# Kernel tuning notes

Measured on AMD Instinct MI355X. Metric: run time of the kernel, lower is better.

The kernel has to match this reference:

```python
import jax, jax.numpy as jnp
import numpy as np

B, N = 65536, 32
Z = jnp.array([0.0, 0.0, 1.0], dtype=jnp.float32)  # joint rotation axis
G = 9.81  # gravity magnitude along +z of base frame (matches base_lin_acc[:,2]=9.81)


def skew(v):
    # [..., 3] -> [..., 3, 3] skew-symmetric matrix
    x, y, z = v[..., 0], v[..., 1], v[..., 2]
    o = jnp.zeros_like(x)
    return jnp.stack([jnp.stack([o, -z, y], -1),
                      jnp.stack([z, o, -x], -1),
                      jnp.stack([-y, x, o], -1)], -2)


def rot_z(q):
    # [B] -> [B, 3, 3] rotation about z (revolute joint)
    c, s = jnp.cos(q), jnp.sin(q)
    o, l = jnp.zeros_like(q), jnp.ones_like(q)
    return jnp.stack([jnp.stack([c, -s, o], -1),
                      jnp.stack([s, c, o], -1),
                      jnp.stack([o, o, l], -1)], -2)


def setup_inputs() -> dict:
    key = jax.random.key(0)
    ks = jax.random.split(key, 8)
    return {
        "q": jax.random.normal(ks[0], (B, N), jnp.float32),
        "qd": jax.random.normal(ks[1], (B, N), jnp.float32),
        "qdd_des": jax.random.normal(ks[2], (B, N), jnp.float32),
        "trans": jax.random.uniform(ks[3], (N, 3), jnp.float32),      # fixed joint-origin offsets
        "mass": jax.random.uniform(ks[4], (N,), jnp.float32) + 0.1,   # positive link masses
        "com": jax.random.uniform(ks[5], (N, 3), jnp.float32),        # center of mass per link
        "inertia": jax.random.normal(ks[6], (N, 3, 3), jnp.float32),  # rotational inertia (about CoM)
        "damping": jax.random.uniform(ks[7], (N,), jnp.float32),      # joint damping consts
    }


def reference(q, qd, qdd_des, trans, mass, com, inertia, damping):
    """Recursive Newton-Euler inverse dynamics (compute_inverse_dynamics),
    for a serial chain of N revolute-z joints, include_gravity=True."""
    Bn = q.shape[0]
    mcom = mass[:, None] * com                                        # [N,3]
    S = skew(com)                                                     # [N,3,3]
    # spatial inertia: I + m * skew(c) @ skew(c)^T (multiply_motion_vec)
    Ibar = inertia + mass[:, None, None] * (S @ jnp.swapaxes(S, -1, -2))

    def fwd_step(carry, xs):
        # propagate velocity/acceleration from parent into child body frame
        v_lin, v_ang, a_lin, a_ang = carry
        qj, qdj, qddj, p = xs
        R = rot_z(qj)                                                 # joint_pose rotation [B,3,3]
        Rt = jnp.swapaxes(R, -1, -2)
        t = -jnp.einsum('bij,j->bi', Rt, p)                           # inverse() translation
        # SpatialMotionVec.transform: ang' = R ang ; lin' = t x ang' + R lin
        wv = jnp.einsum('bij,bj->bi', Rt, v_ang)
        lv = jnp.cross(t, wv) + jnp.einsum('bij,bj->bi', Rt, v_lin)
        wa = jnp.einsum('bij,bj->bi', Rt, a_ang)
        la = jnp.cross(t, wa) + jnp.einsum('bij,bj->bi', Rt, a_lin)
        jv = qdj[:, None] * Z                                         # joint_vel (ang only)
        ja = qddj[:, None] * Z                                        # joint_acc (ang only)
        v_ang_n = wv + jv
        v_lin_n = lv
        # acc = parent_acc + joint_acc + vel x joint_vel (cross_motion_vec)
        a_ang_n = wa + ja + jnp.cross(v_ang_n, jv)
        a_lin_n = la + jnp.cross(v_lin_n, jv)
        c = (v_lin_n, v_ang_n, a_lin_n, a_ang_n)
        return c, (v_lin_n, v_ang_n, a_lin_n, a_ang_n, R)

    zeros3 = jnp.zeros((Bn, 3), q.dtype)
    base_lin_acc = zeros3.at[:, 2].set(jnp.asarray(G, q.dtype))       # gravity as base acc
    init = (zeros3, zeros3, base_lin_acc, zeros3)
    xs = (q.T, qd.T, qdd_des.T, trans)
    _, (v_lin_s, v_ang_s, a_lin_s, a_ang_s, R_s) = jax.lax.scan(fwd_step, init, xs)

    def bwd_step(carry, xs):
        # backward force recursion: f_i = I a_i + v_i x* (I v_i) + X(joint_pose_{i+1}) f_{i+1}
        g_lin, g_ang = carry
        v_lin, v_ang, a_lin, a_ang, R, p, m, mc, Ib = xs
        # inertia.multiply_motion_vec on acc and vel
        fa_lin = m * a_lin + jnp.cross(mc[None, :], a_ang)
        fa_ang = jnp.einsum('ij,bj->bi', Ib, a_ang) + jnp.cross(mc[None, :], a_lin)
        fv_lin = m * v_lin + jnp.cross(mc[None, :], v_ang)
        fv_ang = jnp.einsum('ij,bj->bi', Ib, v_ang) + jnp.cross(mc[None, :], v_lin)
        # vel.cross_force_vec(I v)
        cf_ang = jnp.cross(v_ang, fv_ang) + jnp.cross(v_lin, fv_lin)
        cf_lin = jnp.cross(v_ang, fv_lin)
        f_lin = fa_lin + cf_lin + g_lin
        f_ang = fa_ang + cf_ang + g_ang
        tau = f_ang[:, 2]                                             # force.ang . z_axis
        # SpatialForceVec.transform by this body's joint_pose (into parent frame)
        Rf = jnp.einsum('bij,bj->bi', R, f_lin)
        out_ang = jnp.cross(p[None, :], Rf) + jnp.einsum('bij,bj->bi', R, f_ang)
        return (Rf, out_ang), tau

    xs_b = (v_lin_s, v_ang_s, a_lin_s, a_ang_s, R_s, trans, mass, mcom, Ibar)
    _, taus = jax.lax.scan(bwd_step, (zeros3, zeros3), xs_b, reverse=True)
    # taus: [N, B]; add joint damping term: damping * qd
    return taus.T + damping[None, :] * qd
```

## Files before the change

### kernel.cpp

```cpp
#include <hip/hip_runtime.h>

#define NJ 32
#define BLK 256

typedef float f2 __attribute__((ext_vector_type(2)));
__device__ __forceinline__ f2 mk2(float x, float y){ f2 r; r.x=x; r.y=y; return r; }


#define MODS1 "row_shr:1 row_mask:0xf bank_mask:0xf bound_ctrl:0"
#define MODS2 "row_shr:2 row_mask:0xf bank_mask:0xf bound_ctrl:0"
#define MODS4 "row_shr:4 row_mask:0xf bank_mask:0xf bound_ctrl:0"
#define MODS8 "row_shr:8 row_mask:0xf bank_mask:0xf bound_ctrl:0"
#define MODSB "row_bcast:15 row_mask:0xa bank_mask:0xf"

#define STEP6(m) \
  "v_add_f32_dpp %0, %0, %0 " m "\n\t" \
  "v_add_f32_dpp %1, %1, %1 " m "\n\t" \
  "v_add_f32_dpp %2, %2, %2 " m "\n\t" \
  "v_add_f32_dpp %3, %3, %3 " m "\n\t" \
  "v_add_f32_dpp %4, %4, %4 " m "\n\t" \
  "v_add_f32_dpp %5, %5, %5 " m "\n\t"

#define STEP4(m) \
  "v_add_f32_dpp %0, %0, %0 " m "\n\t" \
  "v_add_f32_dpp %1, %1, %1 " m "\n\t" \
  "v_add_f32_dpp %2, %2, %2 " m "\n\t" \
  "v_add_f32_dpp %3, %3, %3 " m "\n\t"

#define STEP2(m) \
  "v_add_f32_dpp %0, %0, %0 " m "\n\t" \
  "v_add_f32_dpp %1, %1, %1 " m "\n\t" \
  "s_nop 0\n\t"

__device__ __forceinline__ void scan6(float& a, float& b, float& c,
                                      float& d, float& e, float& f) {
    asm("s_nop 1\n\t"
        STEP6(MODS1) STEP6(MODS2) STEP6(MODS4) STEP6(MODS8) STEP6(MODSB)
        : "+v"(a), "+v"(b), "+v"(c), "+v"(d), "+v"(e), "+v"(f));
}

__device__ __forceinline__ void scan4(float& a, float& b, float& c, float& d) {
    asm("s_nop 1\n\t"
        STEP4(MODS1) STEP4(MODS2) STEP4(MODS4) STEP4(MODS8) STEP4(MODSB)
        : "+v"(a), "+v"(b), "+v"(c), "+v"(d));
}

__device__ __forceinline__ void scan2(float& a, float& b) {
    asm("s_nop 1\n\t"
        STEP2(MODS1) STEP2(MODS2) STEP2(MODS4) STEP2(MODS8) STEP2(MODSB)
        : "+v"(a), "+v"(b));
}

__device__ __forceinline__ float seg_total(float x, int hiHalf) {
    int lo, hi;
    asm("s_nop 1\n\t"
        "v_readlane_b32 %0, %2, 31\n\t"
        "v_readlane_b32 %1, %2, 63"
        : "=s"(lo), "=s"(hi) : "v"(x));
    return __int_as_float(hiHalf ? hi : lo);
}

__device__ __forceinline__ float wave_shr1(float x) {
    return __int_as_float(
        __builtin_amdgcn_update_dpp(0, __float_as_int(x), 0x138, 0xf, 0xf, false));
}

__device__ __forceinline__ void fast_sincos(float x, float& s, float& c) {
    float r = __builtin_amdgcn_fractf(x * 0.15915494309189535f);
    s = __builtin_amdgcn_sinf(r);
    c = __builtin_amdgcn_cosf(r);
}

__global__ __launch_bounds__(BLK) void rnea_kernel(
    const float* __restrict__ q,
    const float* __restrict__ qd,
    const float* __restrict__ qdd,
    const float* __restrict__ trans,
    const float* __restrict__ mass,
    const float* __restrict__ com,
    const float* __restrict__ inertia,
    const float* __restrict__ damping,
    float* __restrict__ out,
    int Bn)
{
    const int t    = blockIdx.x * BLK + threadIdx.x;
    const int lane = threadIdx.x & 31;
    const int hiH  = (threadIdx.x >> 5) & 1;
    const int half = Bn >> 1;
    const int r0   = t >> 5;
    if (r0 >= half) return;
    const size_t i0 = (size_t)r0 * NJ + lane;
    const size_t i1 = i0 + (size_t)half * NJ;

    f2 qv   = mk2(q  [i0], q  [i1]);
    f2 qdv  = mk2(qd [i0], qd [i1]);
    f2 qddv = mk2(qdd[i0], qdd[i1]);

    float m    = mass[lane];
    float cx   = com[3*lane+0], cy = com[3*lane+1];
    float mcx  = m*cx, mcy = m*cy;
    float i2zz = fmaf(m, cx*cx + cy*cy, inertia[9*lane+8]);
    float px   = trans[3*lane+0], py = trans[3*lane+1];
    float damp = damping[lane];
    const bool seg0 = (lane == 0);

    float phi0 = qv.x,  phi1 = qv.y;
    float wI0  = qdv.x, wI1  = qdv.y;
    float aI0  = qddv.x, aI1 = qddv.y;
    scan6(phi0, phi1, wI0, wI1, aI0, aI1);
    f2 wI = mk2(wI0, wI1), aI = mk2(aI0, aI1);
    f2 wP = wI - qdv;
    f2 aP = aI - qddv;

    float c0, s0, c1, s1;
    fast_sincos(phi0, s0, c0);
    fast_sincos(phi1, s1, c1);
    f2 c  = mk2(c0, c1), s = mk2(s0, s1);
    f2 cp = mk2(wave_shr1(c0), wave_shr1(c1));
    f2 sp = mk2(wave_shr1(s0), wave_shr1(s1));
    if (seg0) { cp = 1.f; sp = 0.f; }

    f2 dx = cp*px - sp*py;
    f2 dy = sp*px + cp*py;

    f2 ux = -wP*dy, uy = wP*dx;
    float VLx0 = ux.x, VLy0 = uy.x, VLx1 = ux.y, VLy1 = uy.y;
    scan4(VLx0, VLy0, VLx1, VLy1);
    f2 VLx = mk2(VLx0, VLx1), VLy = mk2(VLy0, VLy1);

    f2 gx = qdv*VLy - aP*dy;
    f2 gy = -qdv*VLx + aP*dx;
    float ALx0 = gx.x, ALy0 = gy.x, ALx1 = gx.y, ALy1 = gy.y;
    scan4(ALx0, ALy0, ALx1, ALy1);
    f2 ALx = mk2(ALx0, ALx1), ALy = mk2(ALy0, ALy1);

    f2 mcwx = c*mcx - s*mcy;
    f2 mcwy = s*mcx + c*mcy;

    f2 fv_lx = m*VLx + wI*mcwy;
    f2 fv_ly = m*VLy - wI*mcwx;

    f2 llx = m*ALx + aI*mcwy - wI*fv_ly;
    f2 lly = m*ALy - aI*mcwx + wI*fv_lx;

    float Px0 = llx.x, Py0 = lly.x, Px1 = llx.y, Py1 = lly.y;
    scan4(Px0, Py0, Px1, Py1);
    f2 Px = mk2(Px0, Px1), Py = mk2(Py0, Py1);
    f2 Tx = mk2(seg_total(Px0, hiH), seg_total(Px1, hiH));
    f2 Ty = mk2(seg_total(Py0, hiH), seg_total(Py1, hiH));
    f2 Fx = Tx - Px + llx;
    f2 Fy = Ty - Py + lly;

    f2 a = aI*i2zz + mcwx*ALy - mcwy*ALx + VLx*fv_ly - VLy*fv_lx;
    f2 b = dx*Fy - dy*Fx;
    f2 ab = a + b;
    float Pr0 = ab.x, Pr1 = ab.y;
    scan2(Pr0, Pr1);
    f2 Pr = mk2(Pr0, Pr1);
    f2 Tr = mk2(seg_total(Pr0, hiH), seg_total(Pr1, hiH));
    f2 Nz = Tr - Pr + a;

    f2 tau = damp*qdv + Nz;
    out[i0] = tau.x;
    out[i1] = tau.y;
}

extern "C" void kernel_launch(void* const* d_in, const int* in_sizes, int n_in,
                              void* d_out, int out_size, void* d_ws, size_t ws_size,
                              hipStream_t stream) {
    const float* q       = (const float*)d_in[0];
    const float* qd      = (const float*)d_in[1];
    const float* qdd     = (const float*)d_in[2];
    const float* trans   = (const float*)d_in[3];
    const float* mass    = (const float*)d_in[4];
    const float* com     = (const float*)d_in[5];
    const float* inertia = (const float*)d_in[6];
    const float* damping = (const float*)d_in[7];
    float* out = (float*)d_out;

    int Bn = in_sizes[0] / NJ;
    long long threads = (long long)(Bn/2) * 32;
    int grid = (int)((threads + BLK - 1) / BLK);
    hipLaunchKernelGGL(rnea_kernel, dim3(grid), dim3(BLK), 0, stream,
                       q, qd, qdd, trans, mass, com, inertia, damping, out, Bn);
}
```

Before: 13.50 us.

## Merge dependent wave scans by algebraically rewriting acceleration and torque recurrences

The separate velocity and acceleration prefix scans are folded into one 12-wide scan. The acceleration is rewritten in closed form using prefix sums of w^2*d and a*d together with a prefix of the joint offsets. The force scan and the torque scan are likewise folded into one 6-wide scan by expanding the moment term with prefix positions. This removes serial scan stages and their DPP latency chains, at the cost of extra scanned values and some reassociation that may change rounding. Index arithmetic also switches from 64-bit to 32-bit.

```diff
diff --git a/kernel.cpp b/kernel.cpp
--- a/kernel.cpp
+++ b/kernel.cpp
@@ -13,42 +13,26 @@
 #define MODS8 "row_shr:8 row_mask:0xf bank_mask:0xf bound_ctrl:0"
 #define MODSB "row_bcast:15 row_mask:0xa bank_mask:0xf"
 
-#define STEP6(m) \
-  "v_add_f32_dpp %0, %0, %0 " m "\n\t" \
-  "v_add_f32_dpp %1, %1, %1 " m "\n\t" \
-  "v_add_f32_dpp %2, %2, %2 " m "\n\t" \
-  "v_add_f32_dpp %3, %3, %3 " m "\n\t" \
-  "v_add_f32_dpp %4, %4, %4 " m "\n\t" \
-  "v_add_f32_dpp %5, %5, %5 " m "\n\t"
+#define D(n,m) "v_add_f32_dpp %" #n ", %" #n ", %" #n " " m "\n\t"
 
-#define STEP4(m) \
-  "v_add_f32_dpp %0, %0, %0 " m "\n\t" \
-  "v_add_f32_dpp %1, %1, %1 " m "\n\t" \
-  "v_add_f32_dpp %2, %2, %2 " m "\n\t" \
-  "v_add_f32_dpp %3, %3, %3 " m "\n\t"
+#define STEP12(m) D(0,m) D(1,m) D(2,m) D(3,m) D(4,m) D(5,m) D(6,m) D(7,m) \
+                  D(8,m) D(9,m) D(10,m) D(11,m)
+#define STEP6(m)  D(0,m) D(1,m) D(2,m) D(3,m) D(4,m) D(5,m)
 
-#define STEP2(m) \
-  "v_add_f32_dpp %0, %0, %0 " m "\n\t" \
-  "v_add_f32_dpp %1, %1, %1 " m "\n\t" \
-  "s_nop 0\n\t"
+__device__ __forceinline__ void scan12(float& a, float& b, float& c, float& d,
+                                       float& e, float& f, float& g, float& h,
+                                       float& i, float& j, float& k, float& l) {
+    asm("s_nop 1\n\t"
+        STEP12(MODS1) STEP12(MODS2) STEP12(MODS4) STEP12(MODS8) STEP12(MODSB)
+        : "+v"(a), "+v"(b), "+v"(c), "+v"(d), "+v"(e), "+v"(f),
+          "+v"(g), "+v"(h), "+v"(i), "+v"(j), "+v"(k), "+v"(l));
+}
 
 __device__ __forceinline__ void scan6(float& a, float& b, float& c,
                                       float& d, float& e, float& f) {
     asm("s_nop 1\n\t"
         STEP6(MODS1) STEP6(MODS2) STEP6(MODS4) STEP6(MODS8) STEP6(MODSB)
         : "+v"(a), "+v"(b), "+v"(c), "+v"(d), "+v"(e), "+v"(f));
-}
-
-__device__ __forceinline__ void scan4(float& a, float& b, float& c, float& d) {
-    asm("s_nop 1\n\t"
-        STEP4(MODS1) STEP4(MODS2) STEP4(MODS4) STEP4(MODS8) STEP4(MODSB)
-        : "+v"(a), "+v"(b), "+v"(c), "+v"(d));
-}
-
-__device__ __forceinline__ void scan2(float& a, float& b) {
-    asm("s_nop 1\n\t"
-        STEP2(MODS1) STEP2(MODS2) STEP2(MODS4) STEP2(MODS8) STEP2(MODSB)
-        : "+v"(a), "+v"(b));
 }
 
 __device__ __forceinline__ float seg_total(float x, int hiHalf) {
@@ -89,8 +73,8 @@
     const int half = Bn >> 1;
     const int r0   = t >> 5;
     if (r0 >= half) return;
-    const size_t i0 = (size_t)r0 * NJ + lane;
-    const size_t i1 = i0 + (size_t)half * NJ;
+    const int i0 = r0 * NJ + lane;
+    const int i1 = i0 + half * NJ;
 
     f2 qv   = mk2(q  [i0], q  [i1]);
     f2 qdv  = mk2(qd [i0], qd [i1]);
@@ -123,42 +107,38 @@
     f2 dx = cp*px - sp*py;
     f2 dy = sp*px + cp*py;
 
-    f2 ux = -wP*dy, uy = wP*dx;
-    float VLx0 = ux.x, VLy0 = uy.x, VLx1 = ux.y, VLy1 = uy.y;
-    scan4(VLx0, VLy0, VLx1, VLy1);
+    f2 w2   = wP*wP;
+    f2 ux   = -wP*dy, uy = wP*dx;
+    f2 sxin = w2*dx + aP*dy;
+    f2 syin = w2*dy - aP*dx;
+    float VLx0 = ux.x, VLy0 = uy.x, Sx0 = sxin.x, Sy0 = syin.x, Dx0 = dx.x, Dy0 = dy.x;
+    float VLx1 = ux.y, VLy1 = uy.y, Sx1 = sxin.y, Sy1 = syin.y, Dx1 = dx.y, Dy1 = dy.y;
+    scan12(VLx0, VLy0, Sx0, Sy0, Dx0, Dy0, VLx1, VLy1, Sx1, Sy1, Dx1, Dy1);
     f2 VLx = mk2(VLx0, VLx1), VLy = mk2(VLy0, VLy1);
-
-    f2 gx = qdv*VLy - aP*dy;
-    f2 gy = -qdv*VLx + aP*dx;
-    float ALx0 = gx.x, ALy0 = gy.x, ALx1 = gx.y, ALy1 = gy.y;
-    scan4(ALx0, ALy0, ALx1, ALy1);
-    f2 ALx = mk2(ALx0, ALx1), ALy = mk2(ALy0, ALy1);
+    f2 Dx  = mk2(Dx0, Dx1),   Dy  = mk2(Dy0, Dy1);
+    f2 ALx = wI*VLy - mk2(Sx0, Sx1);
+    f2 ALy = -wI*VLx - mk2(Sy0, Sy1);
 
     f2 mcwx = c*mcx - s*mcy;
     f2 mcwy = s*mcx + c*mcy;
-
     f2 fv_lx = m*VLx + wI*mcwy;
     f2 fv_ly = m*VLy - wI*mcwx;
-
     f2 llx = m*ALx + aI*mcwy - wI*fv_ly;
     f2 lly = m*ALy - aI*mcwx + wI*fv_lx;
+    f2 a = aI*i2zz + mcwx*ALy - mcwy*ALx + VLx*fv_ly - VLy*fv_lx;
+    f2 e = Dx*lly - Dy*llx;
+    f2 g = a + e;
 
-    float Px0 = llx.x, Py0 = lly.x, Px1 = llx.y, Py1 = lly.y;
-    scan4(Px0, Py0, Px1, Py1);
-    f2 Px = mk2(Px0, Px1), Py = mk2(Py0, Py1);
-    f2 Tx = mk2(seg_total(Px0, hiH), seg_total(Px1, hiH));
-    f2 Ty = mk2(seg_total(Py0, hiH), seg_total(Py1, hiH));
-    f2 Fx = Tx - Px + llx;
-    f2 Fy = Ty - Py + lly;
-
-    f2 a = aI*i2zz + mcwx*ALy - mcwy*ALx + VLx*fv_ly - VLy*fv_lx;
-    f2 b = dx*Fy - dy*Fx;
-    f2 ab = a + b;
-    float Pr0 = ab.x, Pr1 = ab.y;
-    scan2(Pr0, Pr1);
-    f2 Pr = mk2(Pr0, Pr1);
-    f2 Tr = mk2(seg_total(Pr0, hiH), seg_total(Pr1, hiH));
-    f2 Nz = Tr - Pr + a;
+    float Plx0 = llx.x, Ply0 = lly.x, Pg0 = g.x;
+    float Plx1 = llx.y, Ply1 = lly.y, Pg1 = g.y;
+    scan6(Plx0, Ply0, Pg0, Plx1, Ply1, Pg1);
+    f2 Tx = mk2(seg_total(Plx0, hiH), seg_total(Plx1, hiH));
+    f2 Ty = mk2(seg_total(Ply0, hiH), seg_total(Ply1, hiH));
+    f2 Tg = mk2(seg_total(Pg0,  hiH), seg_total(Pg1,  hiH));
+    f2 Fx = Tx - mk2(Plx0, Plx1) + llx;
+    f2 Fy = Ty - mk2(Ply0, Ply1) + lly;
+    f2 sg = Tg - mk2(Pg0,  Pg1)  + g;
+    f2 Nz = sg - (Dx*Fy - Dy*Fx);
 
     f2 tau = damp*qdv + Nz;
     out[i0] = tau.x;
```

Measured after the change: 14.27 us. 1.06x slower.
